# Kernel optimization log

Hardware: AMD Instinct MI355X
Metric: run time of the kernel (lower is better)

Reference implementation:

```python
import jax, jax.numpy as jnp
import numpy as np

B, C_IN, C_OUT = 2, 64, 64
NLAT_IN, NLON_IN = 181, 360
NLAT_OUT, NLON_OUT = 181, 360
KERNEL_SIZE = 9            # piecewise-linear basis, kernel_shape=(3,4): (3-1)*4+1
NNZ_PER = 24               # sparse neighbor entries per (kernel fn, output latitude)
NNZ = KERNEL_SIZE * NLAT_OUT * NNZ_PER


def setup_inputs() -> dict:
    key = jax.random.key(0)
    ks = jax.random.split(key, 6)
    x = jax.random.normal(ks[0], (B, C_IN, NLAT_IN, NLON_IN), jnp.float32)
    # quadrature-merged, normalized filter values (positive, O(1/support) scale)
    psi_vals = jax.random.uniform(ks[1], (NNZ,), jnp.float32) / NNZ_PER
    # structured sparse pattern: every (kernel, lat_out) pair has NNZ_PER neighbors
    psi_ker = jnp.repeat(jnp.arange(KERNEL_SIZE, dtype=jnp.int32), NLAT_OUT * NNZ_PER)
    psi_lat_out = jnp.tile(jnp.repeat(jnp.arange(NLAT_OUT, dtype=jnp.int32), NNZ_PER), KERNEL_SIZE)
    dlat = jax.random.randint(ks[2], (NNZ,), -1, 2, dtype=jnp.int32)
    psi_lat_in = jnp.clip(psi_lat_out + dlat, 0, NLAT_IN - 1)
    psi_lon_in = jax.random.randint(ks[3], (NNZ,), 0, NLON_IN, dtype=jnp.int32)
    scale = (1.0 / (C_IN * KERNEL_SIZE)) ** 0.5
    weight = scale * jax.random.normal(ks[4], (C_OUT, C_IN, KERNEL_SIZE), jnp.float32)
    bias = jnp.zeros((C_OUT,), jnp.float32)
    return dict(x=x, psi_vals=psi_vals, weight=weight, bias=bias,
                psi_ker=psi_ker, psi_lat_out=psi_lat_out,
                psi_lat_in=psi_lat_in, psi_lon_in=psi_lon_in)


def _disco_contraction(x, psi_vals, psi_ker, psi_lat_out, psi_lat_in, psi_lon_in):
    """Sparse DISCO contraction: y[b,c,k,lat_out,p] = sum_e psi_vals[e] *
    x[b,c,lat_in_e,(lon_in_e + p*pscale) % nlon_in]  for entries with (k_e, lat_out_e).
    Mirrors torch-harmonics' roll-and-sparse-bmm loop over output longitudes."""
    b, c, nlat_in, nlon_in = x.shape
    pscale = nlon_in // NLON_OUT
    xf = x.reshape(b * c, nlat_in, nlon_in)          # [BC, nlat_in, nlon_in]
    seg = psi_ker * NLAT_OUT + psi_lat_out           # [NNZ] segment id = (k, lat_out)
    nseg = KERNEL_SIZE * NLAT_OUT

    def one_shift(p):
        lon = (psi_lon_in + p * pscale) % nlon_in    # rolled longitude per entry
        g = xf[:, psi_lat_in, lon] * psi_vals        # [BC, NNZ] gather-multiply
        return jax.ops.segment_sum(g.T, seg, num_segments=nseg)  # [nseg, BC]

    ys = jax.lax.map(one_shift, jnp.arange(NLON_OUT))            # [NLON_OUT, nseg, BC]
    y = ys.transpose(1, 0, 2).reshape(KERNEL_SIZE, NLAT_OUT, NLON_OUT, b, c)
    return y.transpose(3, 4, 0, 1, 2)                # [B, C_in, K, nlat_out, nlon_out]


def reference(x, psi_vals, weight, bias, psi_ker, psi_lat_out, psi_lat_in, psi_lon_in):
    y = _disco_contraction(x, psi_vals, psi_ker, psi_lat_out, psi_lat_in, psi_lon_in)
    # groups=1: weight is [C_out, C_in, K]
    out = jnp.einsum("bckxy,fck->bfxy", y, weight)
    out = out + bias[None, :, None, None]
    return out
```

## Files before the change

### kernel.cpp

```cpp
#include <hip/hip_runtime.h>


#define NB    2
#define CIN   64
#define COUT  64
#define KS    9
#define NLAT  181
#define NLON  360
#define NPER  24
#define TP    128

typedef _Float16 f16;
typedef _Float16 f16x8 __attribute__((ext_vector_type(8)));
typedef float    f32x4 __attribute__((ext_vector_type(4)));
typedef unsigned int u32;
typedef unsigned short u16;
typedef u32 u32x4 __attribute__((ext_vector_type(4)));

#define ROWB      23040
#define XT_BYTES  ((size_t)NB * 2 * NLAT * NLON * 32 * 2)
#define WT_BYTES  (KS * 64 * 64 * 2)
#define NMETA     (KS * NLAT * NPER)
#define XS_BYTES  (3 * ROWB)

__global__ __launch_bounds__(384) void prep_kernel(
    const float* __restrict__ x, const float* __restrict__ weight,
    const float* __restrict__ psi_vals, const int* __restrict__ psi_lat_in,
    const int* __restrict__ psi_lon_in,
    f16* __restrict__ xT, f16* __restrict__ wT, int4* __restrict__ meta)
{
    const int tid = threadIdx.x;
    const int lat = blockIdx.x, b = blockIdx.y, z = blockIdx.z;
    if (z == 8) {
        if (b == 0 && lat < 36 && tid < 256) {
            int e0 = lat * 1024 + tid * 4;
#pragma unroll
            for (int u = 0; u < 4; ++u) {
                int e = e0 + u;
                int c = e & 63, f = (e >> 6) & 63, k = e >> 12;
                wT[e] = (f16)weight[((size_t)(f * 64 + c)) * KS + k];
            }
        }
        return;
    }
    if (z == 9) {
        if (b == 0 && lat < 153 && tid < 256) {
            int e = lat * 256 + tid;
            if (e < NMETA) {
                int lt = (e / NPER) % NLAT;
                f16 pvh = (f16)psi_vals[e];
                u32 pb = (u32)__builtin_bit_cast(u16, pvh);
                int lonb = psi_lon_in[e] << 6;
                int4 m;
                m.x = (int)((pb << 16) | pb);
                m.y = (psi_lat_in[e] - lt + 1) * ROWB + lonb;
                m.z = lonb;
                m.w = 0;
                meta[e] = m;
            }
        }
        return;
    }
    if (tid >= NLON) return;
    const int g = z, lon = tid;
    const int h = g >> 2, oh = g & 3;
    const float* src = x + ((size_t)(b * CIN + g * 8) * NLAT + lat) * NLON + lon;
    f16x8 v;
#pragma unroll
    for (int j = 0; j < 8; ++j)
        v[j] = (f16)src[(size_t)j * NLAT * NLON];
    const int op = oh ^ ((lon >> 1) & 3);
    *(f16x8*)&xT[(((size_t)(b * 2 + h) * NLAT + lat) * NLON + lon) * 32 + op * 8] = v;
}

__global__ __launch_bounds__(512, 4) void disco_main(
    const f16* __restrict__ xT, const f16* __restrict__ wT,
    const int4* __restrict__ meta, const float* __restrict__ bias,
    float* __restrict__ out)
{
    extern __shared__ char xs[];
    const int tid  = threadIdx.x;
    const int lane = tid & 63, wave = tid >> 6;
    const int pn   = lane & 15, q = lane >> 4;
    const int pchunk = blockIdx.x, lat = blockIdx.y, b = blockIdx.z;

    const int p  = pchunk * TP + wave * 16 + pn;
    const int pl = p >= NLON ? p - NLON : p;
    const u32 plq  = (u32)((pl << 6) + (q << 4));
    const u32 plqm = plq - (u32)ROWB;
    const u32 thr  = (u32)((NLON - pl) << 6);

    int rr0 = lat > 0 ? lat - 1 : 0;
    int rr2 = lat < NLAT - 1 ? lat + 1 : NLAT - 1;

    f32x4 D[4];
#pragma unroll
    for (int ft = 0; ft < 4; ++ft) D[ft] = (f32x4){0.f, 0.f, 0.f, 0.f};

    for (int h = 0; h < 2; ++h) {
        __syncthreads();
        {
            const size_t hb = (size_t)(b * 2 + h) * NLAT;
            const f16* s0 = xT + (hb + rr0) * NLON * 32;
            const f16* s1 = xT + (hb + lat) * NLON * 32;
            const f16* s2 = xT + (hb + rr2) * NLON * 32;
            for (int i = tid; i < 1440; i += 512) {
                *(f16x8*)&xs[i * 16]             = *(const f16x8*)&s0[i * 8];
                *(f16x8*)&xs[ROWB + i * 16]      = *(const f16x8*)&s1[i * 8];
                *(f16x8*)&xs[2 * ROWB + i * 16]  = *(const f16x8*)&s2[i * 8];
            }
        }
        __syncthreads();

        for (int k = 0; k < KS; ++k) {
            f16x8 acc = (f16x8){0, 0, 0, 0, 0, 0, 0, 0};
            const int4* mp = meta + (k * NLAT + lat) * NPER;
#pragma unroll
            for (int tg = 0; tg < NPER; tg += 8) {
                int4 m[8];
#pragma unroll
                for (int j = 0; j < 8; ++j) m[j] = mp[tg + j];

                u32 addr[8];
#pragma unroll
                for (int j = 0; j < 8; ++j) {
                    u32 ad = ((u32)m[j].z >= thr) ? plqm : plq;
                    u32 a  = (u32)m[j].y + ad;
                    addr[j] = a ^ ((a >> 3) & 48u);
                }
                f16x8 xv[8];
#pragma unroll
                for (int j = 0; j < 8; ++j)
                    xv[j] = *(const f16x8*)(xs + addr[j]);
#pragma unroll
                for (int j = 0; j < 8; ++j) {
                    u32 pk = (u32)m[j].x;
                    u32x4 pkv = {pk, pk, pk, pk};
                    acc += xv[j] * __builtin_bit_cast(f16x8, pkv);
                }
            }

            f16x8 Af[4];
            const f16* wk = wT + (size_t)k * 4096 + h * 32 + q * 8;
#pragma unroll
            for (int ft = 0; ft < 4; ++ft)
                Af[ft] = *(const f16x8*)&wk[(ft * 16 + pn) * 64];
#pragma unroll
            for (int ft = 0; ft < 4; ++ft)
                D[ft] = __builtin_amdgcn_mfma_f32_16x16x32_f16(Af[ft], acc, D[ft], 0, 0, 0);
        }
    }

    if (p < NLON) {
#pragma unroll
        for (int ft = 0; ft < 4; ++ft)
#pragma unroll
            for (int r = 0; r < 4; ++r) {
                const int f = ft * 16 + q * 4 + r;
                out[((size_t)(b * COUT + f) * NLAT + lat) * NLON + p] = D[ft][r] + bias[f];
            }
    }
}

extern "C" void kernel_launch(void* const* d_in, const int* in_sizes, int n_in,
                              void* d_out, int out_size, void* d_ws, size_t ws_size,
                              hipStream_t stream) {
    const float* x          = (const float*)d_in[0];
    const float* psi_vals   = (const float*)d_in[1];
    const float* weight     = (const float*)d_in[2];
    const float* bias       = (const float*)d_in[3];
    const int*   psi_lat_in = (const int*)d_in[6];
    const int*   psi_lon_in = (const int*)d_in[7];
    float* out = (float*)d_out;

    f16*  xT   = (f16*)d_ws;
    f16*  wT   = (f16*)((char*)d_ws + XT_BYTES);
    int4* meta = (int4*)((char*)d_ws + XT_BYTES + WT_BYTES);

    (void)hipFuncSetAttribute((const void*)disco_main,
                              hipFuncAttributeMaxDynamicSharedMemorySize, XS_BYTES);

    prep_kernel<<<dim3(NLAT, NB, 10), 384, 0, stream>>>(
        x, weight, psi_vals, psi_lat_in, psi_lon_in, xT, wT, meta);
    disco_main<<<dim3(3, NLAT, NB), 512, XS_BYTES, stream>>>(
        xT, wT, meta, bias, out);
}
```

Before: 216.7 us.

## Reorder metadata by latitude and broadcast it via wave-wide loads with readlane

```diff
diff --git a/kernel.cpp b/kernel.cpp
--- a/kernel.cpp
+++ b/kernel.cpp
@@ -17,65 +17,65 @@
 typedef unsigned short u16;
 typedef u32 u32x4 __attribute__((ext_vector_type(4)));
 
-#define ROWB      23040
-#define XT_BYTES  ((size_t)NB * 2 * NLAT * NLON * 32 * 2)
-#define WT_BYTES  (KS * 64 * 64 * 2)
-#define NMETA     (KS * NLAT * NPER)
-#define XS_BYTES  (3 * ROWB)
+#define ROWB       23040
+#define XT_BYTES   ((size_t)NB * 2 * NLAT * NLON * 32 * 2)
+#define WT_BYTES   (KS * 64 * 64 * 2)
+#define NMETA      (KS * NLAT * NPER)
+#define META_BYTES ((size_t)NMETA * 16 + 256)
+#define XS_BYTES   (3 * ROWB)
 
 __global__ __launch_bounds__(384) void prep_kernel(
     const float* __restrict__ x, const float* __restrict__ weight,
     const float* __restrict__ psi_vals, const int* __restrict__ psi_lat_in,
     const int* __restrict__ psi_lon_in,
-    f16* __restrict__ xT, f16* __restrict__ wT, int4* __restrict__ meta)
+    f16* __restrict__ xT, f16* __restrict__ wT, int4* __restrict__ metaR)
 {
     const int tid = threadIdx.x;
-    const int lat = blockIdx.x, b = blockIdx.y, z = blockIdx.z;
-    if (z == 8) {
-        if (b == 0 && lat < 36 && tid < 256) {
-            int e0 = lat * 1024 + tid * 4;
+    const int bx = blockIdx.x, b = blockIdx.y;
+    if (bx < NLAT) {
+        if (tid >= NLON) return;
+        const int lat = bx, lon = tid;
+        const int sw = (lon >> 1) & 3;
 #pragma unroll
-            for (int u = 0; u < 4; ++u) {
-                int e = e0 + u;
-                int c = e & 63, f = (e >> 6) & 63, k = e >> 12;
-                wT[e] = (f16)weight[((size_t)(f * 64 + c)) * KS + k];
-            }
+        for (int g = 0; g < 8; ++g) {
+            const float* src = x + ((size_t)(b * CIN + g * 8) * NLAT + lat) * NLON + lon;
+            f16x8 v;
+#pragma unroll
+            for (int j = 0; j < 8; ++j)
+                v[j] = (f16)src[(size_t)j * NLAT * NLON];
+            const int op = (g & 3) ^ sw;
+            *(f16x8*)&xT[(((size_t)(b * 2 + (g >> 2)) * NLAT + lat) * NLON + lon) * 32
+                         + op * 8] = v;
         }
         return;
     }
-    if (z == 9) {
-        if (b == 0 && lat < 153 && tid < 256) {
-            int e = lat * 256 + tid;
-            if (e < NMETA) {
-                int lt = (e / NPER) % NLAT;
-                f16 pvh = (f16)psi_vals[e];
-                u32 pb = (u32)__builtin_bit_cast(u16, pvh);
-                int lonb = psi_lon_in[e] << 6;
-                int4 m;
-                m.x = (int)((pb << 16) | pb);
-                m.y = (psi_lat_in[e] - lt + 1) * ROWB + lonb;
-                m.z = lonb;
-                m.w = 0;
-                meta[e] = m;
-            }
+    if (bx == NLAT) {
+        for (int e = b * 384 + tid; e < KS * 64 * 64; e += 768) {
+            int c = e & 63, f = (e >> 6) & 63, k = e >> 12;
+            wT[e] = (f16)weight[((size_t)(f * 64 + c)) * KS + k];
         }
         return;
     }
-    if (tid >= NLON) return;
-    const int g = z, lon = tid;
-    const int h = g >> 2, oh = g & 3;
-    const float* src = x + ((size_t)(b * CIN + g * 8) * NLAT + lat) * NLON + lon;
-    f16x8 v;
-#pragma unroll
-    for (int j = 0; j < 8; ++j)
-        v[j] = (f16)src[(size_t)j * NLAT * NLON];
-    const int op = oh ^ ((lon >> 1) & 3);
-    *(f16x8*)&xT[(((size_t)(b * 2 + h) * NLAT + lat) * NLON + lon) * 32 + op * 8] = v;
+    int w = ((bx - (NLAT + 1)) * 2 + b) * 384 + tid;
+    for (int o = w; o < NMETA; o += 1536) {
+        int lat = o / 216, r = o - lat * 216;
+        int k = r / 24, t = r - k * 24;
+        int e = (k * NLAT + lat) * NPER + t;
+        f16 pvh = (f16)psi_vals[e];
+        u32 pb = (u32)__builtin_bit_cast(u16, pvh);
+        int lonb = psi_lon_in[e] << 6;
+        int4 m;
+        m.x = (int)((pb << 16) | pb);
+        m.y = (psi_lat_in[e] - lat + 1) * ROWB + lonb;
+        m.z = lonb;
+        m.w = 0;
+        metaR[o] = m;
+    }
 }
 
 __global__ __launch_bounds__(512, 4) void disco_main(
     const f16* __restrict__ xT, const f16* __restrict__ wT,
-    const int4* __restrict__ meta, const float* __restrict__ bias,
+    const int* __restrict__ metaI, const float* __restrict__ bias,
     float* __restrict__ out)
 {
     extern __shared__ char xs[];
@@ -97,6 +97,8 @@
 #pragma unroll
     for (int ft = 0; ft < 4; ++ft) D[ft] = (f32x4){0.f, 0.f, 0.f, 0.f};
 
+    const int* mi = metaI + lat * 864;
+
     for (int h = 0; h < 2; ++h) {
         __syncthreads();
         {
@@ -113,20 +115,31 @@
         __syncthreads();
 
         for (int k = 0; k < KS; ++k) {
+            const int kb = k * 96;
+            const u32 vm0 = (u32)mi[kb + lane];
+            const u32 vm1 = (u32)mi[kb + 64 + lane];
+
             f16x8 acc = (f16x8){0, 0, 0, 0, 0, 0, 0, 0};
-            const int4* mp = meta + (k * NLAT + lat) * NPER;
 #pragma unroll
             for (int tg = 0; tg < NPER; tg += 8) {
-                int4 m[8];
-#pragma unroll
-                for (int j = 0; j < 8; ++j) m[j] = mp[tg + j];
-
-                u32 addr[8];
+                u32 addr[8], pks[8];
 #pragma unroll
                 for (int j = 0; j < 8; ++j) {
-                    u32 ad = ((u32)m[j].z >= thr) ? plqm : plq;
-                    u32 a  = (u32)m[j].y + ad;
+                    const int t = tg + j, off = 4 * t;
+                    u32 pk, my, mz;
+                    if (off < 64) {
+                        pk = (u32)__builtin_amdgcn_readlane((int)vm0, off);
+                        my = (u32)__builtin_amdgcn_readlane((int)vm0, off + 1);
+                        mz = (u32)__builtin_amdgcn_readlane((int)vm0, off + 2);
+                    } else {
+                        pk = (u32)__builtin_amdgcn_readlane((int)vm1, off - 64);
+                        my = (u32)__builtin_amdgcn_readlane((int)vm1, off - 63);
+                        mz = (u32)__builtin_amdgcn_readlane((int)vm1, off - 62);
+                    }
+                    u32 ad = (mz >= thr) ? plqm : plq;
+                    u32 a  = my + ad;
                     addr[j] = a ^ ((a >> 3) & 48u);
+                    pks[j]  = pk;
                 }
                 f16x8 xv[8];
 #pragma unroll
@@ -134,8 +147,7 @@
                     xv[j] = *(const f16x8*)(xs + addr[j]);
 #pragma unroll
                 for (int j = 0; j < 8; ++j) {
-                    u32 pk = (u32)m[j].x;
-                    u32x4 pkv = {pk, pk, pk, pk};
+                    u32x4 pkv = {pks[j], pks[j], pks[j], pks[j]};
                     acc += xv[j] * __builtin_bit_cast(f16x8, pkv);
                 }
             }
@@ -173,15 +185,15 @@
     const int*   psi_lon_in = (const int*)d_in[7];
     float* out = (float*)d_out;
 
-    f16*  xT   = (f16*)d_ws;
-    f16*  wT   = (f16*)((char*)d_ws + XT_BYTES);
-    int4* meta = (int4*)((char*)d_ws + XT_BYTES + WT_BYTES);
+    f16*  xT    = (f16*)d_ws;
+    f16*  wT    = (f16*)((char*)d_ws + XT_BYTES);
+    int4* metaR = (int4*)((char*)d_ws + XT_BYTES + WT_BYTES);
 
     (void)hipFuncSetAttribute((const void*)disco_main,
                               hipFuncAttributeMaxDynamicSharedMemorySize, XS_BYTES);
 
-    prep_kernel<<<dim3(NLAT, NB, 10), 384, 0, stream>>>(
-        x, weight, psi_vals, psi_lat_in, psi_lon_in, xT, wT, meta);
+    prep_kernel<<<dim3(NLAT + 3, NB), 384, 0, stream>>>(
+        x, weight, psi_vals, psi_lat_in, psi_lon_in, xT, wT, metaR);
     disco_main<<<dim3(3, NLAT, NB), 512, XS_BYTES, stream>>>(
-        xT, wT, meta, bias, out);
+        xT, wT, (const int*)metaR, bias, out);
 }
```

New measurement: 224.4 us. 3.6% more time.

## Retile main kernel to two 12-wave blocks per row and flatten prep grid

Applied to the files above, without the earlier changes.

```diff
diff --git a/kernel.cpp b/kernel.cpp
--- a/kernel.cpp
+++ b/kernel.cpp
@@ -8,7 +8,6 @@
 #define NLAT  181
 #define NLON  360
 #define NPER  24
-#define TP    128
 
 typedef _Float16 f16;
 typedef _Float16 f16x8 __attribute__((ext_vector_type(8)));
@@ -23,57 +22,63 @@
 #define NMETA     (KS * NLAT * NPER)
 #define XS_BYTES  (3 * ROWB)
 
-__global__ __launch_bounds__(384) void prep_kernel(
+#define U0  (NB * 2 * 4 * NLAT * NLON)
+#define G0  ((U0 + 255) / 256)
+#define G1  ((KS * 4096 + 255) / 256)
+#define G2  ((NMETA + 255) / 256)
+
+__global__ __launch_bounds__(256) void prep_kernel(
     const float* __restrict__ x, const float* __restrict__ weight,
     const float* __restrict__ psi_vals, const int* __restrict__ psi_lat_in,
     const int* __restrict__ psi_lon_in,
     f16* __restrict__ xT, f16* __restrict__ wT, int4* __restrict__ meta)
 {
-    const int tid = threadIdx.x;
-    const int lat = blockIdx.x, b = blockIdx.y, z = blockIdx.z;
-    if (z == 8) {
-        if (b == 0 && lat < 36 && tid < 256) {
-            int e0 = lat * 1024 + tid * 4;
+    const int bid = blockIdx.x, tid = threadIdx.x;
+    if (bid < G0) {
+        const int u = bid * 256 + tid;
+        if (u >= U0) return;
+        const int oct = u & 3;
+        const int v   = u >> 2;
+        const int lon = v % NLON;
+        const int w   = v / NLON;
+        const int lat = w % NLAT;
+        const int z   = w / NLAT;
+        const int h   = z & 1, b = z >> 1;
+        const float* src = x + ((size_t)(b * CIN + h * 32 + oct * 8) * NLAT + lat) * NLON + lon;
+        f16x8 vv;
 #pragma unroll
-            for (int u = 0; u < 4; ++u) {
-                int e = e0 + u;
-                int c = e & 63, f = (e >> 6) & 63, k = e >> 12;
-                wT[e] = (f16)weight[((size_t)(f * 64 + c)) * KS + k];
-            }
+        for (int j = 0; j < 8; ++j)
+            vv[j] = (f16)src[(size_t)j * NLAT * NLON];
+        const int op = oct ^ ((lon >> 1) & 3);
+        *(f16x8*)&xT[(((size_t)z * NLAT + lat) * NLON + lon) * 32 + op * 8] = vv;
+        return;
+    }
+    if (bid < G0 + G1) {
+        const int e = (bid - G0) * 256 + tid;
+        if (e < KS * 4096) {
+            int c = e & 63, f = (e >> 6) & 63, k = e >> 12;
+            wT[e] = (f16)weight[((size_t)(f * 64 + c)) * KS + k];
         }
         return;
     }
-    if (z == 9) {
-        if (b == 0 && lat < 153 && tid < 256) {
-            int e = lat * 256 + tid;
-            if (e < NMETA) {
-                int lt = (e / NPER) % NLAT;
-                f16 pvh = (f16)psi_vals[e];
-                u32 pb = (u32)__builtin_bit_cast(u16, pvh);
-                int lonb = psi_lon_in[e] << 6;
-                int4 m;
-                m.x = (int)((pb << 16) | pb);
-                m.y = (psi_lat_in[e] - lt + 1) * ROWB + lonb;
-                m.z = lonb;
-                m.w = 0;
-                meta[e] = m;
-            }
+    {
+        const int e = (bid - G0 - G1) * 256 + tid;
+        if (e < NMETA) {
+            int lat = (e / NPER) % NLAT;
+            f16 pvh = (f16)psi_vals[e];
+            u32 pb = (u32)__builtin_bit_cast(u16, pvh);
+            int lonb = psi_lon_in[e] << 6;
+            int4 m;
+            m.x = (int)((pb << 16) | pb);
+            m.y = (psi_lat_in[e] - lat + 1) * ROWB + lonb;
+            m.z = lonb;
+            m.w = 0;
+            meta[e] = m;
         }
-        return;
     }
-    if (tid >= NLON) return;
-    const int g = z, lon = tid;
-    const int h = g >> 2, oh = g & 3;
-    const float* src = x + ((size_t)(b * CIN + g * 8) * NLAT + lat) * NLON + lon;
-    f16x8 v;
-#pragma unroll
-    for (int j = 0; j < 8; ++j)
-        v[j] = (f16)src[(size_t)j * NLAT * NLON];
-    const int op = oh ^ ((lon >> 1) & 3);
-    *(f16x8*)&xT[(((size_t)(b * 2 + h) * NLAT + lat) * NLON + lon) * 32 + op * 8] = v;
 }
 
-__global__ __launch_bounds__(512, 4) void disco_main(
+__global__ __launch_bounds__(768, 6) void disco_main(
     const f16* __restrict__ xT, const f16* __restrict__ wT,
     const int4* __restrict__ meta, const float* __restrict__ bias,
     float* __restrict__ out)
@@ -82,9 +87,11 @@
     const int tid  = threadIdx.x;
     const int lane = tid & 63, wave = tid >> 6;
     const int pn   = lane & 15, q = lane >> 4;
-    const int pchunk = blockIdx.x, lat = blockIdx.y, b = blockIdx.z;
+    const int half2 = blockIdx.x, lat = blockIdx.y, b = blockIdx.z;
 
-    const int p  = pchunk * TP + wave * 16 + pn;
+    const int tile = half2 * 12 + wave;
+    const bool act = tile < 23;
+    const int p  = tile * 16 + pn;
     const int pl = p >= NLON ? p - NLON : p;
     const u32 plq  = (u32)((pl << 6) + (q << 4));
     const u32 plqm = plq - (u32)ROWB;
@@ -104,7 +111,7 @@
             const f16* s0 = xT + (hb + rr0) * NLON * 32;
             const f16* s1 = xT + (hb + lat) * NLON * 32;
             const f16* s2 = xT + (hb + rr2) * NLON * 32;
-            for (int i = tid; i < 1440; i += 512) {
+            for (int i = tid; i < 1440; i += 768) {
                 *(f16x8*)&xs[i * 16]             = *(const f16x8*)&s0[i * 8];
                 *(f16x8*)&xs[ROWB + i * 16]      = *(const f16x8*)&s1[i * 8];
                 *(f16x8*)&xs[2 * ROWB + i * 16]  = *(const f16x8*)&s2[i * 8];
@@ -112,46 +119,48 @@
         }
         __syncthreads();
 
-        for (int k = 0; k < KS; ++k) {
-            f16x8 acc = (f16x8){0, 0, 0, 0, 0, 0, 0, 0};
-            const int4* mp = meta + (k * NLAT + lat) * NPER;
+        if (act) {
+            for (int k = 0; k < KS; ++k) {
+                f16x8 acc = (f16x8){0, 0, 0, 0, 0, 0, 0, 0};
+                const int4* mp = meta + (k * NLAT + lat) * NPER;
 #pragma unroll
-            for (int tg = 0; tg < NPER; tg += 8) {
-                int4 m[8];
+                for (int tg = 0; tg < NPER; tg += 8) {
+                    int4 m[8];
 #pragma unroll
-                for (int j = 0; j < 8; ++j) m[j] = mp[tg + j];
+                    for (int j = 0; j < 8; ++j) m[j] = mp[tg + j];
 
-                u32 addr[8];
+                    u32 addr[8];
 #pragma unroll
-                for (int j = 0; j < 8; ++j) {
-                    u32 ad = ((u32)m[j].z >= thr) ? plqm : plq;
-                    u32 a  = (u32)m[j].y + ad;
-                    addr[j] = a ^ ((a >> 3) & 48u);
+                    for (int j = 0; j < 8; ++j) {
+                        u32 ad = ((u32)m[j].z >= thr) ? plqm : plq;
+                        u32 a  = (u32)m[j].y + ad;
+                        addr[j] = a ^ ((a >> 3) & 48u);
+                    }
+                    f16x8 xv[8];
+#pragma unroll
+                    for (int j = 0; j < 8; ++j)
+                        xv[j] = *(const f16x8*)(xs + addr[j]);
+#pragma unroll
+                    for (int j = 0; j < 8; ++j) {
+                        u32 pk = (u32)m[j].x;
+                        u32x4 pkv = {pk, pk, pk, pk};
+                        acc += xv[j] * __builtin_bit_cast(f16x8, pkv);
+                    }
                 }
-                f16x8 xv[8];
+
+                f16x8 Af[4];
+                const f16* wk = wT + (size_t)k * 4096 + h * 32 + q * 8;
 #pragma unroll
-                for (int j = 0; j < 8; ++j)
-                    xv[j] = *(const f16x8*)(xs + addr[j]);
+                for (int ft = 0; ft < 4; ++ft)
+                    Af[ft] = *(const f16x8*)&wk[(ft * 16 + pn) * 64];
 #pragma unroll
-                for (int j = 0; j < 8; ++j) {
-                    u32 pk = (u32)m[j].x;
-                    u32x4 pkv = {pk, pk, pk, pk};
-                    acc += xv[j] * __builtin_bit_cast(f16x8, pkv);
-                }
+                for (int ft = 0; ft < 4; ++ft)
+                    D[ft] = __builtin_amdgcn_mfma_f32_16x16x32_f16(Af[ft], acc, D[ft], 0, 0, 0);
             }
-
-            f16x8 Af[4];
-            const f16* wk = wT + (size_t)k * 4096 + h * 32 + q * 8;
-#pragma unroll
-            for (int ft = 0; ft < 4; ++ft)
-                Af[ft] = *(const f16x8*)&wk[(ft * 16 + pn) * 64];
-#pragma unroll
-            for (int ft = 0; ft < 4; ++ft)
-                D[ft] = __builtin_amdgcn_mfma_f32_16x16x32_f16(Af[ft], acc, D[ft], 0, 0, 0);
         }
     }
 
-    if (p < NLON) {
+    if (act && p < NLON) {
 #pragma unroll
         for (int ft = 0; ft < 4; ++ft)
 #pragma unroll
@@ -180,8 +189,8 @@
     (void)hipFuncSetAttribute((const void*)disco_main,
                               hipFuncAttributeMaxDynamicSharedMemorySize, XS_BYTES);
 
-    prep_kernel<<<dim3(NLAT, NB, 10), 384, 0, stream>>>(
+    prep_kernel<<<dim3(G0 + G1 + G2), 256, 0, stream>>>(
         x, weight, psi_vals, psi_lat_in, psi_lon_in, xT, wT, meta);
-    disco_main<<<dim3(3, NLAT, NB), 512, XS_BYTES, stream>>>(
+    disco_main<<<dim3(2, NLAT, NB), 768, XS_BYTES, stream>>>(
         xT, wT, meta, bias, out);
 }
```

Result: faster. 191.7 us (-11.5%).
